# Performance work log

Hardware: AMD Instinct MI355X
Metric: run time of the kernel (lower is better)

The kernel has to match this reference:

```python
import jax, jax.numpy as jnp
import numpy as np

B, S, HS = 2, 2048, 4096
NH, NKV = 32, 32
HD = HS // NH
INTER = 11008
VOCAB = 32000
EPS = 1e-6
ROPE_BASE = 10000.0


def setup_inputs() -> dict:
    key = jax.random.key(0)
    ks = jax.random.split(key, 16)
    sc = 0.02
    return {
        "hidden_states": jax.random.normal(ks[0], (B, S, HS), jnp.float32),
        "input_ids": jax.random.randint(ks[1], (B, S), 0, VOCAB, jnp.int32),
        "position_ids": jnp.arange(S, dtype=jnp.int32)[None, :],
        "embed": jax.random.normal(ks[2], (VOCAB, HS), jnp.float32) * sc,
        "fc_w": jax.random.normal(ks[3], (HS, 2 * HS), jnp.float32) * sc,
        "fc_b": jnp.zeros((HS,), jnp.float32),
        "q_w": jax.random.normal(ks[4], (NH * HD, HS), jnp.float32) * sc,
        "k_w": jax.random.normal(ks[5], (NKV * HD, HS), jnp.float32) * sc,
        "v_w": jax.random.normal(ks[6], (NKV * HD, HS), jnp.float32) * sc,
        "o_w": jax.random.normal(ks[7], (HS, NH * HD), jnp.float32) * sc,
        "gate_w": jax.random.normal(ks[8], (INTER, HS), jnp.float32) * sc,
        "up_w": jax.random.normal(ks[9], (INTER, HS), jnp.float32) * sc,
        "down_w": jax.random.normal(ks[10], (HS, INTER), jnp.float32) * sc,
        "post_ln_w": jnp.ones((HS,), jnp.float32),
    }


def _rotate_half(x):
    x1, x2 = jnp.split(x, 2, axis=-1)
    return jnp.concatenate((-x2, x1), axis=-1)


def _rms_norm(x, w, eps=EPS):
    x32 = x.astype(jnp.float32)
    x32 = x32 * jax.lax.rsqrt(jnp.mean(x32 * x32, axis=-1, keepdims=True) + eps)
    return (w * x32).astype(x.dtype)


def _forward(hidden_states, input_ids, position_ids, embed, fc_w, fc_b,
             q_w, k_w, v_w, o_w, gate_w, up_w, down_w, post_ln_w):
    # Embedding lookup (detached in original via no_grad)
    embeds = jax.lax.stop_gradient(embed[input_ids])  # [B,S,HS]
    h = jnp.concatenate((embeds, hidden_states), axis=-1) @ fc_w.T + fc_b  # [B,S,HS]

    # --- decoder layer 0 (no input_layernorm) ---
    residual = h
    q = (h @ q_w.T).reshape(B, S, NH, HD).transpose(0, 2, 1, 3)   # [B,NH,S,HD]
    k = (h @ k_w.T).reshape(B, S, NKV, HD).transpose(0, 2, 1, 3)
    v = (h @ v_w.T).reshape(B, S, NKV, HD).transpose(0, 2, 1, 3)

    # RoPE
    pos = position_ids[0].astype(jnp.float32)                      # [S]
    inv_freq = 1.0 / (ROPE_BASE ** (jnp.arange(0, HD, 2, dtype=jnp.float32) / HD))
    freqs = pos[:, None] * inv_freq[None, :]                       # [S,HD/2]
    emb = jnp.concatenate((freqs, freqs), axis=-1)                 # [S,HD]
    cos = jnp.cos(emb)[None, None, :, :]
    sin = jnp.sin(emb)[None, None, :, :]
    q = q * cos + _rotate_half(q) * sin
    k = k * cos + _rotate_half(k) * sin

    # attention (num_kv_groups == 1 here)
    scores = jnp.einsum('bhqd,bhkd->bhqk', q, k) / np.sqrt(HD)     # [B,NH,S,S]
    causal = jnp.triu(jnp.ones((S, S), bool), 1)
    scores = jnp.where(causal[None, None], -jnp.inf, scores)
    attn = jax.nn.softmax(scores.astype(jnp.float32), axis=-1).astype(q.dtype)
    out = jnp.einsum('bhqk,bhkd->bhqd', attn, v)                   # [B,NH,S,HD]
    out = out.transpose(0, 2, 1, 3).reshape(B, S, HS)
    attn_out = out @ o_w.T

    h = residual + attn_out
    residual = h
    hn = _rms_norm(h, post_ln_w)
    mlp = (jax.nn.silu(hn @ gate_w.T) * (hn @ up_w.T)) @ down_w.T
    return residual + mlp


def reference(hidden_states, input_ids, position_ids, embed, fc_w, fc_b,
              q_w, k_w, v_w, o_w, gate_w, up_w, down_w, post_ln_w):
    return _forward(hidden_states, input_ids, position_ids, embed, fc_w, fc_b,
                    q_w, k_w, v_w, o_w, gate_w, up_w, down_w, post_ln_w)
```

## Files before the change

kernel.cpp:

```cpp
#include <hip/hip_runtime.h>
#include <hip/hip_bf16.h>

typedef __attribute__((ext_vector_type(8))) short short8;
typedef __attribute__((ext_vector_type(4))) short short4v;
typedef __attribute__((ext_vector_type(4))) float floatx4;

#define B_SZ 2
#define S_SZ 2048
#define HS_SZ 4096
#define NH_SZ 32
#define HD_SZ 128
#define INTER_SZ 11008
#define M_TOT 4096

__device__ __forceinline__ float b2f(short s){
  unsigned int u = ((unsigned int)(unsigned short)s) << 16;
  return __builtin_bit_cast(float, u);
}
__device__ __forceinline__ short f2b(float f){
  unsigned int u = __builtin_bit_cast(unsigned int, f);
  u = (u + 0x7FFFu + ((u >> 16) & 1u)) >> 16;
  return (short)u;
}

typedef __attribute__((address_space(1))) const unsigned int gu32;
typedef __attribute__((address_space(3))) unsigned int lu32;
__device__ __forceinline__ void gl2lds16(const short* g, short* l){
  __builtin_amdgcn_global_load_lds((gu32*)g, (lu32*)l, 16, 0, 0);
}

#define BARRIER() asm volatile("s_barrier" ::: "memory")
#define WAITV8()  asm volatile("s_waitcnt vmcnt(8)" ::: "memory")
#define WAITV0()  asm volatile("s_waitcnt vmcnt(0)" ::: "memory")

__global__ void cvt_bf16_kernel(const float* __restrict__ src, short* __restrict__ dst, long n8){
  long idx = (long)blockIdx.x * blockDim.x + threadIdx.x;
  if (idx >= n8) return;
  long e = idx * 8;
  floatx4 v0 = *(const floatx4*)(src + e);
  floatx4 v1 = *(const floatx4*)(src + e + 4);
  short8 o;
  o[0]=f2b(v0[0]); o[1]=f2b(v0[1]); o[2]=f2b(v0[2]); o[3]=f2b(v0[3]);
  o[4]=f2b(v1[0]); o[5]=f2b(v1[1]); o[6]=f2b(v1[2]); o[7]=f2b(v1[3]);
  *(short8*)(dst + e) = o;
}

__global__ void embed_concat_kernel(const float* __restrict__ hidden,
                                    const int* __restrict__ ids,
                                    const float* __restrict__ embed,
                                    short* __restrict__ X0){
  long idx = (long)blockIdx.x * blockDim.x + threadIdx.x;
  const long total = (long)M_TOT * (2*HS_SZ) / 4;
  if (idx >= total) return;
  long e = idx * 4;
  int m = (int)(e / (2*HS_SZ));
  int c = (int)(e % (2*HS_SZ));
  const float* src;
  if (c < HS_SZ){
    src = embed + (long)ids[m]*HS_SZ + c;
  } else {
    src = hidden + (long)m*HS_SZ + (c - HS_SZ);
  }
  floatx4 v = *(const floatx4*)src;
  short4v o;
  o[0]=f2b(v[0]); o[1]=f2b(v[1]); o[2]=f2b(v[2]); o[3]=f2b(v[3]);
  *(short4v*)(X0 + e) = o;
}

template<int EPI>
__global__ __launch_bounds__(512, 2)
void gemm256_kernel(const short* __restrict__ A, const short* __restrict__ Bw,
                    int M, int N, int K,
                    const float* __restrict__ bias,
                    const float* __restrict__ resid,
                    short* __restrict__ Cbf,
                    float* __restrict__ Cf){
  __shared__ __align__(16) short lds[65536];
  const int tid = threadIdx.x;
  const int wid = tid >> 6;
  const int lane = tid & 63;
  const int wr = wid >> 2, wc = wid & 3;
  const int lr = lane & 15, lk = lane >> 4;
  const int lr7 = lr & 7;

  const int nwg = gridDim.x * gridDim.y;
  const int id  = blockIdx.y * gridDim.x + blockIdx.x;
  const int cpx = nwg >> 3;
  const int sw  = (id & 7) * cpx + (id >> 3);
  const int bx  = sw % gridDim.x;
  const int by  = sw / gridDim.x;
  const int m0 = bx * 256, n0 = by * 256;

  const int srow = lane >> 3;
  const int sslot = (lane & 7) ^ srow;
  const short* gsrc[8];
  int ldsoff[8];
  #pragma unroll
  for (int op=0; op<2; op++)
    #pragma unroll
    for (int h=0; h<2; h++)
      #pragma unroll
      for (int i=0; i<2; i++){
        const int u = op*4 + h*2 + i;
        const int seg = wid*2 + i;
        const int row = (op ? n0 : m0) + h*128 + seg*8 + srow;
        gsrc[u] = (op ? Bw : A) + (long)row*K + sslot*8;
        ldsoff[u] = op*16384 + h*8192 + seg*512;
      }

  floatx4 acc[8][4] = {};
  int a_base[8], b_base[4];
  #pragma unroll
  for (int mf=0; mf<8; mf++) a_base[mf] = (wr*128 + mf*16 + lr)*64;
  #pragma unroll
  for (int nf=0; nf<4; nf++) b_base[nf] = 16384 + (wc*64 + nf*16 + lr)*64;
  const int kslot[2] = { ((0*4+lk)^lr7)*8, ((1*4+lk)^lr7)*8 };

  const int nt = K >> 6;

  #pragma unroll
  for (int u=0; u<8; u++) gl2lds16(gsrc[u], lds + ldsoff[u]);

  for (int t=0; t<nt; ++t){
    const int dbase = (t & 1) * 32768;
    const int nbase = ((t+1) & 1) * 32768;
    if (t+1 < nt){
      const long kn = (long)(t+1) * 64;
      #pragma unroll
      for (int u=0; u<8; u++) gl2lds16(gsrc[u] + kn, lds + nbase + ldsoff[u]);
      WAITV8();
    } else {
      WAITV0();
    }
    BARRIER();
    short8 bfr[4][2];
    #pragma unroll
    for (int q=0; q<4; q++){
      short8 af[2][2];
      #pragma unroll
      for (int p=0; p<2; p++){
        const int ab = dbase + a_base[q*2+p];
        af[p][0] = *(const short8*)(lds + ab + kslot[0]);
        af[p][1] = *(const short8*)(lds + ab + kslot[1]);
      }
      if (q == 0){
        #pragma unroll
        for (int nf=0; nf<4; nf++){
          const int bb = dbase + b_base[nf];
          bfr[nf][0] = *(const short8*)(lds + bb + kslot[0]);
          bfr[nf][1] = *(const short8*)(lds + bb + kslot[1]);
        }
      }
      __builtin_amdgcn_s_setprio(1);
      #pragma unroll
      for (int p=0; p<2; p++){
        #pragma unroll
        for (int nf=0; nf<4; nf++){
          acc[q*2+p][nf] = __builtin_amdgcn_mfma_f32_16x16x32_bf16(af[p][0], bfr[nf][0], acc[q*2+p][nf], 0,0,0);
          acc[q*2+p][nf] = __builtin_amdgcn_mfma_f32_16x16x32_bf16(af[p][1], bfr[nf][1], acc[q*2+p][nf], 0,0,0);
        }
      }
      __builtin_amdgcn_s_setprio(0);
    }
    BARRIER();
  }

  #pragma unroll
  for (int mf=0; mf<8; mf++){
    #pragma unroll
    for (int nf=0; nf<4; nf++){
      const int col = n0 + wc*64 + nf*16 + lr;
      float bcol = (EPI==1) ? bias[col] : 0.0f;
      #pragma unroll
      for (int r=0; r<4; r++){
        const int row = m0 + wr*128 + mf*16 + lk*4 + r;
        float v = acc[mf][nf][r] + bcol;
        if (EPI==2) v += resid[(long)row*N + col];
        if (EPI==0 || EPI==1) Cbf[(long)row*N + col] = f2b(v);
        if (EPI==1 || EPI==2) Cf[(long)row*N + col] = v;
      }
    }
  }
}

__global__ void rope_kernel(short* __restrict__ q, short* __restrict__ k,
                            const int* __restrict__ pos_ids){
  long idx = (long)blockIdx.x * blockDim.x + threadIdx.x;
  const long total = (long)M_TOT * NH_SZ * (HD_SZ/2);
  if (idx >= total) return;
  int i  = (int)(idx & 63);
  long rh = idx >> 6;
  int h  = (int)(rh & 31);
  int m  = (int)(rh >> 5);
  int s  = m & (S_SZ - 1);
  float p = (float)pos_ids[s];
  const float L2_10000 = 13.28771237954945f;
  float inv = exp2f(-(2.0f*i/(float)HD_SZ) * L2_10000);
  float fr = p * inv;
  float sn, cs;
  sincosf(fr, &sn, &cs);
  long base = (long)m*HS_SZ + h*HD_SZ;
  short* qp = q + base;
  short* kp = k + base;
  float q1=b2f(qp[i]), q2=b2f(qp[i+64]);
  qp[i]    = f2b(q1*cs - q2*sn);
  qp[i+64] = f2b(q2*cs + q1*sn);
  float k1=b2f(kp[i]), k2=b2f(kp[i+64]);
  kp[i]    = f2b(k1*cs - k2*sn);
  kp[i+64] = f2b(k2*cs + k1*sn);
}

__global__ __launch_bounds__(256)
void vtrans_kernel(const short* __restrict__ V, short* __restrict__ VT){
  __shared__ short tile[64][68];
  const int s0 = blockIdx.x * 64;
  const int d0 = blockIdx.y * 64;
  const int bh = blockIdx.z;
  const int b = bh >> 5, h = bh & 31;
  const int tid = threadIdx.x;
  #pragma unroll
  for (int it=0; it<2; it++){
    int e = (it*256 + tid) * 8;
    int ss = e >> 6, col = e & 63;
    short8 v = *(const short8*)(V + ((long)(b*S_SZ + s0 + ss))*HS_SZ + h*HD_SZ + d0 + col);
    #pragma unroll
    for (int j=0;j<8;j++) tile[ss][col+j] = v[j];
  }
  __syncthreads();
  #pragma unroll
  for (int it=0; it<2; it++){
    int e = (it*256 + tid) * 8;
    int dd = e >> 6, scol = e & 63;
    short8 w;
    #pragma unroll
    for (int j=0;j<8;j++) w[j] = tile[scol+j][dd];
    *(short8*)(VT + ((long)(bh*HD_SZ + d0 + dd))*S_SZ + s0 + scol) = w;
  }
}

__global__ __launch_bounds__(256,2)
void attn_kernel(const short* __restrict__ Q, const short* __restrict__ K,
                 const short* __restrict__ VT, short* __restrict__ O){
  constexpr int LPD = 72;
  __shared__ __align__(16) short lds[32768];
  __shared__ __align__(16) short p_lds[4][16*LPD];
  const int bh = blockIdx.y;
  const int b = bh >> 5, h = bh & 31;
  const int q0 = blockIdx.x * 64;
  const int tid = threadIdx.x, wid = tid>>6, lane = tid&63;
  const int lr = lane & 15, lk = lane >> 4;
  const float scale = 0.08838834764831845f;

  const short* qbase = Q + ((long)(b*S_SZ + q0 + wid*16))*HS_SZ + h*HD_SZ;
  short8 qf[4];
  #pragma unroll
  for (int t=0;t<4;t++)
    qf[t] = *(const short8*)(qbase + (long)lr*HS_SZ + t*32 + lk*8);

  const short* kb[4]; const short* vb[4];
  int kloff[4], vloff[4];
  #pragma unroll
  for (int p=0;p<4;p++){
    const int seg = wid*4 + p;
    const int rowk = seg*4 + (lane >> 4);
    const int slotk = (lane & 15) ^ (rowk & 15);
    kb[p] = K + ((long)(b*S_SZ) + rowk)*HS_SZ + h*HD_SZ + slotk*8;
    kloff[p] = seg*512;
    const int dv = seg*8 + (lane >> 3);
    const int slotv = (lane & 7) ^ (dv & 7);
    vb[p] = VT + ((long)(bh*HD_SZ + dv))*S_SZ + slotv*8;
    vloff[p] = 8192 + seg*512;
  }

  floatx4 oacc[8] = {};
  float m_run[4] = {-1e30f,-1e30f,-1e30f,-1e30f};
  float l_run[4] = {0.f,0.f,0.f,0.f};

  const int nt = blockIdx.x + 1;

  #pragma unroll
  for (int p=0;p<4;p++){
    gl2lds16(kb[p], lds + kloff[p]);
    gl2lds16(vb[p], lds + vloff[p]);
  }

  for (int t=0; t<nt; ++t){
    const int dbase = (t & 1) * 16384;
    const int nbase = ((t+1) & 1) * 16384;
    if (t+1 < nt){
      const long kkn = (long)(t+1)*64*HS_SZ;
      const long vkn = (long)(t+1)*64;
      #pragma unroll
      for (int p=0;p<4;p++){
        gl2lds16(kb[p] + kkn, lds + nbase + kloff[p]);
        gl2lds16(vb[p] + vkn, lds + nbase + vloff[p]);
      }
      WAITV8();
    } else {
      WAITV0();
    }
    BARRIER();
    const int kv0 = t*64;
    floatx4 sfr[4];
    #pragma unroll
    for (int fn=0; fn<4; fn++){
      floatx4 s = {0.f,0.f,0.f,0.f};
      const int row = fn*16 + lr;
      #pragma unroll
      for (int tq=0; tq<4; tq++){
        short8 kf = *(const short8*)(lds + dbase + row*128 + (((tq*4+lk)^lr)&15)*8);
        s = __builtin_amdgcn_mfma_f32_16x16x32_bf16(qf[tq], kf, s, 0,0,0);
      }
      sfr[fn] = s;
    }
    float pv[4][4];
    #pragma unroll
    for (int fn=0; fn<4; fn++){
      const int col = kv0 + fn*16 + lr;
      #pragma unroll
      for (int r=0;r<4;r++){
        const int row = q0 + wid*16 + lk*4 + r;
        float sv = sfr[fn][r] * scale;
        pv[fn][r] = (col > row) ? -1e30f : sv;
      }
    }
    float mr4[4];
    int small = 1;
    #pragma unroll
    for (int r=0;r<4;r++){
      float mr = fmaxf(fmaxf(pv[0][r], pv[1][r]), fmaxf(pv[2][r], pv[3][r]));
      mr = fmaxf(mr, __shfl_xor(mr, 1, 16));
      mr = fmaxf(mr, __shfl_xor(mr, 2, 16));
      mr = fmaxf(mr, __shfl_xor(mr, 4, 16));
      mr = fmaxf(mr, __shfl_xor(mr, 8, 16));
      mr4[r] = mr;
      small &= (mr <= m_run[r] + 8.0f) ? 1 : 0;
    }
    const int skip = __all(small);
    float alpha_[4];
    #pragma unroll
    for (int r=0;r<4;r++){
      float mnew = skip ? m_run[r] : fmaxf(m_run[r], mr4[r]);
      alpha_[r] = skip ? 1.0f : __expf(m_run[r] - mnew);
      m_run[r] = mnew;
      float rs = 0.f;
      #pragma unroll
      for (int fn=0; fn<4; fn++){
        float e = __expf(pv[fn][r] - mnew);
        p_lds[wid][(lk*4+r)*LPD + fn*16 + lr] = f2b(e);
        rs += e;
      }
      rs += __shfl_xor(rs, 1, 16);
      rs += __shfl_xor(rs, 2, 16);
      rs += __shfl_xor(rs, 4, 16);
      rs += __shfl_xor(rs, 8, 16);
      l_run[r] = l_run[r]*alpha_[r] + rs;
    }
    if (!skip){
      #pragma unroll
      for (int f=0; f<8; f++){
        #pragma unroll
        for (int r=0;r<4;r++) oacc[f][r] *= alpha_[r];
      }
    }
    short8 pf[2];
    #pragma unroll
    for (int tp=0; tp<2; tp++)
      pf[tp] = *(const short8*)(&p_lds[wid][lr*LPD + tp*32 + lk*8]);
    #pragma unroll
    for (int f=0; f<8; f++){
      const int vrow = f*16 + lr;
      #pragma unroll
      for (int tp=0; tp<2; tp++){
        short8 vf = *(const short8*)(lds + dbase + 8192 + vrow*64 + (((tp*4+lk)^(lr&7))&7)*8);
        oacc[f] = __builtin_amdgcn_mfma_f32_16x16x32_bf16(pf[tp], vf, oacc[f], 0,0,0);
      }
    }
    BARRIER();
  }
  #pragma unroll
  for (int r=0;r<4;r++){
    const float inv = 1.0f / l_run[r];
    const long row = (long)(b*S_SZ + q0 + wid*16 + lk*4 + r);
    #pragma unroll
    for (int f=0; f<8; f++){
      O[row*HS_SZ + h*HD_SZ + f*16 + lr] = f2b(oacc[f][r]*inv);
    }
  }
}

__global__ void rmsnorm_kernel(const float* __restrict__ X, const float* __restrict__ W,
                               short* __restrict__ Y){
  const int row = blockIdx.x;
  const float* x = X + (long)row*HS_SZ;
  float ss = 0.f;
  for (int c = threadIdx.x*4; c < HS_SZ; c += 256*4){
    floatx4 v = *(const floatx4*)(x + c);
    ss += v[0]*v[0] + v[1]*v[1] + v[2]*v[2] + v[3]*v[3];
  }
  ss += __shfl_xor(ss, 32); ss += __shfl_xor(ss, 16);
  ss += __shfl_xor(ss, 8);  ss += __shfl_xor(ss, 4);
  ss += __shfl_xor(ss, 2);  ss += __shfl_xor(ss, 1);
  __shared__ float red[4];
  if ((threadIdx.x & 63) == 0) red[threadIdx.x >> 6] = ss;
  __syncthreads();
  ss = red[0] + red[1] + red[2] + red[3];
  const float rs = rsqrtf(ss / (float)HS_SZ + 1e-6f);
  for (int c = threadIdx.x*4; c < HS_SZ; c += 256*4){
    floatx4 v = *(const floatx4*)(x + c);
    floatx4 w = *(const floatx4*)(W + c);
    short4v o;
    o[0]=f2b(v[0]*rs*w[0]); o[1]=f2b(v[1]*rs*w[1]);
    o[2]=f2b(v[2]*rs*w[2]); o[3]=f2b(v[3]*rs*w[3]);
    *(short4v*)(Y + (long)row*HS_SZ + c) = o;
  }
}

__global__ void silu_mul_kernel(short* __restrict__ G, const short* __restrict__ U){
  long idx = (long)blockIdx.x * blockDim.x + threadIdx.x;
  const long total = (long)M_TOT * INTER_SZ / 8;
  if (idx >= total) return;
  long e = idx * 8;
  short8 g = *(short8*)(G + e);
  short8 u = *(const short8*)(U + e);
  short8 o;
  #pragma unroll
  for (int j=0;j<8;j++){
    float gf = b2f(g[j]);
    float uf = b2f(u[j]);
    float s = gf / (1.0f + __expf(-gf));
    o[j] = f2b(s * uf);
  }
  *(short8*)(G + e) = o;
}

extern "C" void kernel_launch(void* const* d_in, const int* in_sizes, int n_in,
                              void* d_out, int out_size, void* d_ws, size_t ws_size,
                              hipStream_t stream){
  (void)in_sizes; (void)n_in; (void)out_size;
  const float* hidden = (const float*)d_in[0];
  const int*   ids    = (const int*)d_in[1];
  const int*   pos    = (const int*)d_in[2];
  const float* embed  = (const float*)d_in[3];
  const float* fc_w   = (const float*)d_in[4];
  const float* fc_b   = (const float*)d_in[5];
  const float* q_w    = (const float*)d_in[6];
  const float* k_w    = (const float*)d_in[7];
  const float* v_w    = (const float*)d_in[8];
  const float* o_w    = (const float*)d_in[9];
  const float* gate_w = (const float*)d_in[10];
  const float* up_w   = (const float*)d_in[11];
  const float* down_w = (const float*)d_in[12];
  const float* ln_w   = (const float*)d_in[13];

  char* ws = (char*)d_ws;
  size_t off = 0;
  auto alloc = [&](size_t bytes)->char*{
    char* p = ws + off;
    off = (off + bytes + 255) & ~(size_t)255;
    return p;
  };
  short* wbf  = (short*)alloc((size_t)INTER_SZ*HS_SZ*2);
  short* X0   = (short*)alloc((size_t)M_TOT*2*HS_SZ*2);
  short* h_bf = (short*)alloc((size_t)M_TOT*HS_SZ*2);
  float* h_f  = (float*)alloc((size_t)M_TOT*HS_SZ*4);
  short* q_bf = (short*)alloc((size_t)M_TOT*HS_SZ*2);
  short* k_bf = (short*)alloc((size_t)M_TOT*HS_SZ*2);
  short* v_bf = (short*)alloc((size_t)M_TOT*HS_SZ*2);
  short* vt_bf= (short*)alloc((size_t)M_TOT*HS_SZ*2);
  short* a_bf = (short*)alloc((size_t)M_TOT*HS_SZ*2);
  float* h2_f = (float*)alloc((size_t)M_TOT*HS_SZ*4);
  short* hn_bf= (short*)alloc((size_t)M_TOT*HS_SZ*2);
  short* g_bf = (short*)alloc((size_t)M_TOT*INTER_SZ*2);
  short* u_bf = (short*)alloc((size_t)M_TOT*INTER_SZ*2);
  if (ws_size < off) return;

  auto cvt = [&](const float* src, short* dst, long n){
    long n8 = n / 8;
    cvt_bf16_kernel<<<(int)((n8 + 255)/256), 256, 0, stream>>>(src, dst, n8);
  };

  embed_concat_kernel<<<32768, 256, 0, stream>>>(hidden, ids, embed, X0);

  cvt(fc_w, wbf, (long)HS_SZ*2*HS_SZ);
  gemm256_kernel<1><<<dim3(16,16), 512, 0, stream>>>(X0, wbf, M_TOT, HS_SZ, 2*HS_SZ,
                                                     fc_b, nullptr, h_bf, h_f);
  cvt(q_w, wbf, (long)HS_SZ*HS_SZ);
  gemm256_kernel<0><<<dim3(16,16), 512, 0, stream>>>(h_bf, wbf, M_TOT, HS_SZ, HS_SZ,
                                                     nullptr, nullptr, q_bf, nullptr);
  cvt(k_w, wbf, (long)HS_SZ*HS_SZ);
  gemm256_kernel<0><<<dim3(16,16), 512, 0, stream>>>(h_bf, wbf, M_TOT, HS_SZ, HS_SZ,
                                                     nullptr, nullptr, k_bf, nullptr);
  cvt(v_w, wbf, (long)HS_SZ*HS_SZ);
  gemm256_kernel<0><<<dim3(16,16), 512, 0, stream>>>(h_bf, wbf, M_TOT, HS_SZ, HS_SZ,
                                                     nullptr, nullptr, v_bf, nullptr);
  rope_kernel<<<32768, 256, 0, stream>>>(q_bf, k_bf, pos);
  vtrans_kernel<<<dim3(S_SZ/64, HD_SZ/64, B_SZ*NH_SZ), 256, 0, stream>>>(v_bf, vt_bf);
  attn_kernel<<<dim3(S_SZ/64, B_SZ*NH_SZ), 256, 0, stream>>>(q_bf, k_bf, vt_bf, a_bf);
  cvt(o_w, wbf, (long)HS_SZ*HS_SZ);
  gemm256_kernel<2><<<dim3(16,16), 512, 0, stream>>>(a_bf, wbf, M_TOT, HS_SZ, HS_SZ,
                                                     nullptr, h_f, nullptr, h2_f);
  rmsnorm_kernel<<<M_TOT, 256, 0, stream>>>(h2_f, ln_w, hn_bf);
  cvt(gate_w, wbf, (long)INTER_SZ*HS_SZ);
  gemm256_kernel<0><<<dim3(16,43), 512, 0, stream>>>(hn_bf, wbf, M_TOT, INTER_SZ, HS_SZ,
                                                     nullptr, nullptr, g_bf, nullptr);
  cvt(up_w, wbf, (long)INTER_SZ*HS_SZ);
  gemm256_kernel<0><<<dim3(16,43), 512, 0, stream>>>(hn_bf, wbf, M_TOT, INTER_SZ, HS_SZ,
                                                     nullptr, nullptr, u_bf, nullptr);
  silu_mul_kernel<<<22016, 256, 0, stream>>>(g_bf, u_bf);
  cvt(down_w, wbf, (long)HS_SZ*INTER_SZ);
  gemm256_kernel<2><<<dim3(16,16), 512, 0, stream>>>(g_bf, wbf, M_TOT, HS_SZ, INTER_SZ,
                                                     nullptr, h2_f, nullptr, (float*)d_out);
}
```

Before: 2.546 ms.

## Switch GEMM mainloop to 4-stage K=32 LDS pipeline without swizzle

Reworks the 256x256 bf16 GEMM main loop from a double-buffered K=64 tile with XOR-swizzled LDS layout to a four-buffer ring of K=32 tiles, keeping three loads in flight. Each stage issues four direct global-to-LDS loads per thread, and the MFMA loop reads unswizzled rows of 32 elements. The deeper prefetch is meant to hide global memory latency better. In exchange there are twice as many barriers per K, and dropping the swizzle risks LDS bank conflicts, since a 64-byte row stride puts lanes on the same banks.

Measured after the change: 2.689 ms. 5.6% more time.

```diff
diff --git a/kernel.cpp b/kernel.cpp
--- a/kernel.cpp
+++ b/kernel.cpp
@@ -31,6 +31,7 @@
 
 #define BARRIER() asm volatile("s_barrier" ::: "memory")
 #define WAITV8()  asm volatile("s_waitcnt vmcnt(8)" ::: "memory")
+#define WAITV4()  asm volatile("s_waitcnt vmcnt(4)" ::: "memory")
 #define WAITV0()  asm volatile("s_waitcnt vmcnt(0)" ::: "memory")
 
 __global__ void cvt_bf16_kernel(const float* __restrict__ src, short* __restrict__ dst, long n8){
@@ -81,7 +82,6 @@
   const int lane = tid & 63;
   const int wr = wid >> 2, wc = wid & 3;
   const int lr = lane & 15, lk = lane >> 4;
-  const int lr7 = lr & 7;
 
   const int nwg = gridDim.x * gridDim.y;
   const int id  = blockIdx.y * gridDim.x + blockIdx.x;
@@ -91,77 +91,46 @@
   const int by  = sw / gridDim.x;
   const int m0 = bx * 256, n0 = by * 256;
 
-  const int srow = lane >> 3;
-  const int sslot = (lane & 7) ^ srow;
-  const short* gsrc[8];
-  int ldsoff[8];
-  #pragma unroll
-  for (int op=0; op<2; op++)
-    #pragma unroll
-    for (int h=0; h<2; h++)
-      #pragma unroll
-      for (int i=0; i<2; i++){
-        const int u = op*4 + h*2 + i;
-        const int seg = wid*2 + i;
-        const int row = (op ? n0 : m0) + h*128 + seg*8 + srow;
-        gsrc[u] = (op ? Bw : A) + (long)row*K + sslot*8;
-        ldsoff[u] = op*16384 + h*8192 + seg*512;
-      }
+  const int srow = wid*16 + (lane >> 2);
+  const int scol = (lane & 3) * 8;
+  const short* ga0 = A  + (long)(m0 + srow)*K + scol;
+  const short* ga1 = A  + (long)(m0 + 128 + srow)*K + scol;
+  const short* gb0 = Bw + (long)(n0 + srow)*K + scol;
+  const short* gb1 = Bw + (long)(n0 + 128 + srow)*K + scol;
 
   floatx4 acc[8][4] = {};
-  int a_base[8], b_base[4];
-  #pragma unroll
-  for (int mf=0; mf<8; mf++) a_base[mf] = (wr*128 + mf*16 + lr)*64;
-  #pragma unroll
-  for (int nf=0; nf<4; nf++) b_base[nf] = 16384 + (wc*64 + nf*16 + lr)*64;
-  const int kslot[2] = { ((0*4+lk)^lr7)*8, ((1*4+lk)^lr7)*8 };
-
-  const int nt = K >> 6;
-
-  #pragma unroll
-  for (int u=0; u<8; u++) gl2lds16(gsrc[u], lds + ldsoff[u]);
-
-  for (int t=0; t<nt; ++t){
-    const int dbase = (t & 1) * 32768;
-    const int nbase = ((t+1) & 1) * 32768;
-    if (t+1 < nt){
-      const long kn = (long)(t+1) * 64;
-      #pragma unroll
-      for (int u=0; u<8; u++) gl2lds16(gsrc[u] + kn, lds + nbase + ldsoff[u]);
-      WAITV8();
-    } else {
-      WAITV0();
-    }
+  const int nt = K >> 5;
+
+  auto stage = [&](int t){
+    const long kk = (long)t * 32;
+    short* db = lds + ((t & 3) * 16384) + wid*512;
+    gl2lds16(ga0 + kk, db);
+    gl2lds16(ga1 + kk, db + 4096);
+    gl2lds16(gb0 + kk, db + 8192);
+    gl2lds16(gb1 + kk, db + 12288);
+  };
+
+  stage(0); stage(1); stage(2);
+
+  for (int t = 0; t < nt; ++t){
+    if (t + 3 < nt) stage(t + 3);
+    if (t + 2 < nt)      { WAITV8(); }
+    else if (t + 1 < nt) { WAITV4(); }
+    else                 { WAITV0(); }
     BARRIER();
-    short8 bfr[4][2];
-    #pragma unroll
-    for (int q=0; q<4; q++){
-      short8 af[2][2];
-      #pragma unroll
-      for (int p=0; p<2; p++){
-        const int ab = dbase + a_base[q*2+p];
-        af[p][0] = *(const short8*)(lds + ab + kslot[0]);
-        af[p][1] = *(const short8*)(lds + ab + kslot[1]);
-      }
-      if (q == 0){
-        #pragma unroll
-        for (int nf=0; nf<4; nf++){
-          const int bb = dbase + b_base[nf];
-          bfr[nf][0] = *(const short8*)(lds + bb + kslot[0]);
-          bfr[nf][1] = *(const short8*)(lds + bb + kslot[1]);
-        }
-      }
-      __builtin_amdgcn_s_setprio(1);
-      #pragma unroll
-      for (int p=0; p<2; p++){
-        #pragma unroll
-        for (int nf=0; nf<4; nf++){
-          acc[q*2+p][nf] = __builtin_amdgcn_mfma_f32_16x16x32_bf16(af[p][0], bfr[nf][0], acc[q*2+p][nf], 0,0,0);
-          acc[q*2+p][nf] = __builtin_amdgcn_mfma_f32_16x16x32_bf16(af[p][1], bfr[nf][1], acc[q*2+p][nf], 0,0,0);
-        }
-      }
-      __builtin_amdgcn_s_setprio(0);
-    }
+    const short* sb = lds + (t & 3) * 16384;
+    short8 bfr[4], af[8];
+    #pragma unroll
+    for (int j=0;j<4;j++) bfr[j] = *(const short8*)(sb + 8192 + (wc*64 + j*16 + lr)*32 + lk*8);
+    #pragma unroll
+    for (int i=0;i<8;i++) af[i]  = *(const short8*)(sb + (wr*128 + i*16 + lr)*32 + lk*8);
+    __builtin_amdgcn_s_setprio(1);
+    #pragma unroll
+    for (int i=0;i<8;i++)
+      #pragma unroll
+      for (int j=0;j<4;j++)
+        acc[i][j] = __builtin_amdgcn_mfma_f32_16x16x32_bf16(af[i], bfr[j], acc[i][j], 0,0,0);
+    __builtin_amdgcn_s_setprio(0);
     BARRIER();
   }
 
```
